# Kernel optimization log

Measured on AMD Instinct MI355X. Metric: run time of the kernel, lower is better.

The kernel has to match this reference:

```python
import jax, jax.numpy as jnp
import numpy as np

B, S, D = 8, 4096, 512      # batch, seq_len, input_dim
H = 2048                    # expert hidden dim
O = 512                     # expert_output_dim
E = 8                       # num_experts
TOP_K = 1


def setup_inputs() -> dict:
    key = jax.random.key(0)
    ks = jax.random.split(key, 8)
    sc = 0.02
    return {
        "x": jax.random.normal(ks[0], (B, S, D), dtype=jnp.float32),
        "Wr": jax.random.normal(ks[1], (D, E), dtype=jnp.float32) * sc,
        "br": jnp.zeros((E,), dtype=jnp.float32),
        "W1": jax.random.normal(ks[2], (E, D, H), dtype=jnp.float32) * sc,
        "b1": jnp.zeros((E, H), dtype=jnp.float32),
        "W2": jax.random.normal(ks[3], (E, H, O), dtype=jnp.float32) * sc,
        "b2": jnp.zeros((E, O), dtype=jnp.float32),
    }


def reference(x, Wr, br, W1, b1, W2, b2):
    b, s, d = x.shape
    xf = x.reshape(-1, d)                                   # [T, D]
    router_logits = xf @ Wr + br                            # [T, E]
    topk_logits, topk_idx = jax.lax.top_k(router_logits, TOP_K)  # [T, K]
    topk_gates = jax.nn.softmax(topk_logits, axis=1)        # [T, K] (ones for K=1)

    out = jnp.zeros((xf.shape[0], O), dtype=x.dtype)
    for k in range(TOP_K):
        idx_k = topk_idx[:, k]                              # [T]
        gate_k = topk_gates[:, k:k + 1]                     # [T, 1]
        # loop over the small fixed expert set; mask-combine per token
        for e in range(E):
            h = jax.nn.relu(xf @ W1[e] + b1[e])             # [T, H]
            oe = h @ W2[e] + b2[e]                          # [T, O]
            mask = (idx_k == e)[:, None]                    # [T, 1]
            out = out + jnp.where(mask, gate_k * oe, 0.0)
    return out.reshape(b, s, O)
```

## Files before the change

### kernel.cpp

```cpp
#include <hip/hip_runtime.h>
#include <stdint.h>

#define N_TOK 32768
#define D_IN  512
#define H_DIM 2048
#define O_DIM 512
#define N_EXP 8
#define NTILES 272
#define TPX    34

typedef __bf16 bf16x8 __attribute__((ext_vector_type(8)));
typedef float  f32x4  __attribute__((ext_vector_type(4)));
typedef unsigned int u32x4 __attribute__((ext_vector_type(4)));

struct alignas(8) us4 { unsigned short x, y, z, w; };

#define FENCE() asm volatile("" ::: "memory")
#define BAR()   do { FENCE(); __builtin_amdgcn_s_barrier(); FENCE(); } while (0)
#define WAITV0  asm volatile("s_waitcnt vmcnt(0)" ::: "memory")

__device__ __forceinline__ unsigned short f2bf(float f) {
  union { float f; unsigned u; } v; v.f = f;
  unsigned r = v.u + 0x7FFFu + ((v.u >> 16) & 1u);
  return (unsigned short)(r >> 16);
}

__device__ __forceinline__ void gll16(const void* src, void* lds_dst) {
  __builtin_amdgcn_global_load_lds(
      (const __attribute__((address_space(1))) void*)src,
      (__attribute__((address_space(3))) void*)lds_dst, 16, 0, 0);
}

__global__ void k_init(int* counts) {
  if (threadIdx.x < N_EXP) counts[threadIdx.x] = 0;
}

__global__ void k_transpose(const float* __restrict__ W, unsigned short* __restrict__ WT,
                            int R, int C) {
  __shared__ unsigned short tile[64][72];
  int e = blockIdx.y;
  const float* src = W + (size_t)e * R * C;
  unsigned short* dst = WT + (size_t)e * R * C;
  int tilesC = C >> 6;
  int tc = (blockIdx.x % tilesC) << 6;
  int tr = (blockIdx.x / tilesC) << 6;
  int tid = threadIdx.x;
  int rq = tid >> 4;
  int cq = tid & 15;
#pragma unroll
  for (int q = 0; q < 4; ++q) {
    int r = q * 16 + rq;
    float4 v = *(const float4*)(src + (size_t)(tr + r) * C + tc + cq * 4);
    us4 b;
    b.x = f2bf(v.x); b.y = f2bf(v.y); b.z = f2bf(v.z); b.w = f2bf(v.w);
    *(us4*)&tile[r][cq * 4] = b;
  }
  __syncthreads();
#pragma unroll
  for (int q = 0; q < 4; ++q) {
    int cc = q * 16 + rq;
    int rr = cq * 4;
    us4 o;
    o.x = tile[rr + 0][cc]; o.y = tile[rr + 1][cc];
    o.z = tile[rr + 2][cc]; o.w = tile[rr + 3][cc];
    *(us4*)(dst + (size_t)(tc + cc) * R + tr + rr) = o;
  }
}

__global__ void k_router(const float* __restrict__ x, const float* __restrict__ Wr,
                         const float* __restrict__ br, int* __restrict__ expert_id,
                         unsigned short* __restrict__ xbf) {
  int token = blockIdx.x * 4 + (threadIdx.x >> 6);
  int lane  = threadIdx.x & 63;
  const float* xr = x + (size_t)token * D_IN;
  float acc[N_EXP];
#pragma unroll
  for (int e = 0; e < N_EXP; ++e) acc[e] = 0.f;
#pragma unroll
  for (int j = 0; j < 2; ++j) {
    int i0 = lane * 8 + j * 4;
    float4 xv = *(const float4*)(xr + i0);
    us4 bb;
    bb.x = f2bf(xv.x); bb.y = f2bf(xv.y); bb.z = f2bf(xv.z); bb.w = f2bf(xv.w);
    *(us4*)(xbf + (size_t)token * D_IN + i0) = bb;
    float xs[4] = {xv.x, xv.y, xv.z, xv.w};
#pragma unroll
    for (int u = 0; u < 4; ++u) {
      const float4* wr = (const float4*)(Wr + (size_t)(i0 + u) * N_EXP);
      float4 w0 = wr[0], w1 = wr[1];
      acc[0] += xs[u] * w0.x; acc[1] += xs[u] * w0.y;
      acc[2] += xs[u] * w0.z; acc[3] += xs[u] * w0.w;
      acc[4] += xs[u] * w1.x; acc[5] += xs[u] * w1.y;
      acc[6] += xs[u] * w1.z; acc[7] += xs[u] * w1.w;
    }
  }
#pragma unroll
  for (int off = 32; off > 0; off >>= 1) {
#pragma unroll
    for (int e = 0; e < N_EXP; ++e) acc[e] += __shfl_xor(acc[e], off, 64);
  }
  if (lane == 0) {
    float best = acc[0] + br[0]; int bi = 0;
#pragma unroll
    for (int e = 1; e < N_EXP; ++e) {
      float v = acc[e] + br[e];
      if (v > best) { best = v; bi = e; }
    }
    expert_id[token] = bi;
  }
}

__global__ void k_count(const int* __restrict__ expert_id, int* __restrict__ counts) {
  __shared__ int lcnt[N_EXP];
  int tid = threadIdx.x;
  if (tid < N_EXP) lcnt[tid] = 0;
  __syncthreads();
  int e = expert_id[blockIdx.x * 1024 + tid];
  atomicAdd(&lcnt[e], 1);
  __syncthreads();
  if (tid < N_EXP) atomicAdd(&counts[tid], lcnt[tid]);
}

__global__ void k_scan(const int* __restrict__ counts, int* __restrict__ offsets,
                       int* __restrict__ cursor, int2* __restrict__ table) {
  int i = threadIdx.x;
  int s = 0, ts = 0, myexp = -1, myt = -1;
#pragma unroll
  for (int e = 0; e < N_EXP; ++e) {
    int c = counts[e];
    int tc = (c + 127) >> 7;
    if (i == e) { offsets[e] = s; cursor[e] = s; }
    if (i >= ts && i < ts + tc) { myexp = e; myt = i - ts; }
    s += c; ts += tc;
  }
  if (i < NTILES) table[i] = make_int2(myexp, myt);
}

__global__ void k_scatter(const int* __restrict__ expert_id, int* __restrict__ cursor,
                          int* __restrict__ idx_list) {
  __shared__ int lcnt[N_EXP], lbase[N_EXP];
  int tid = threadIdx.x;
  int i = blockIdx.x * 512 + tid;
  if (tid < N_EXP) lcnt[tid] = 0;
  __syncthreads();
  int e = expert_id[i];
  int lpos = atomicAdd(&lcnt[e], 1);
  __syncthreads();
  if (tid < N_EXP) lbase[tid] = atomicAdd(&cursor[tid], lcnt[tid]);
  __syncthreads();
  idx_list[lbase[e] + lpos] = i;
}


__launch_bounds__(256, 4)
__global__ void k_gemm1(const unsigned short* __restrict__ xbf,
                        const unsigned short* __restrict__ W1T,
                        const float* __restrict__ b1,
                        const int* __restrict__ counts, const int* __restrict__ offsets,
                        const int2* __restrict__ table, const int* __restrict__ idx_list,
                        unsigned short* __restrict__ Hperm,
                        int nt1, int ch, int hchunk) {
  int xcd = blockIdx.x & 7;
  int s   = blockIdx.x >> 3;
  int tile  = xcd * TPX + s / nt1;
  int ntile = s % nt1;
  int2 et = table[tile];
  int e = et.x;
  if (e < 0) return;
  int base   = offsets[e] + et.y * 128;
  int mvalid = min(128, counts[e] - et.y * 128);

  __shared__ __align__(16) unsigned char lds[32768];

  int tid = threadIdx.x, w = tid >> 6, lane = tid & 63;
  int l15 = lane & 15, l4 = lane >> 4;
  int wr = w >> 1, wc = w & 1;
  int n0 = ch * hchunk + ntile * 128;

  unsigned offA[4], offB[4];
#pragma unroll
  for (int q = 0; q < 4; ++q) {
    int d   = q * 4096 + w * 1024 + lane * 16;
    int row = d >> 7;
    int bs  = (d & 127) ^ ((row & 7) << 4);
    int tok = idx_list[base + min(row, mvalid - 1)];
    offA[q] = (unsigned)tok * (D_IN * 2) + bs;
    offB[q] = (unsigned)(e * H_DIM + n0 + row) * (D_IN * 2) + bs;
  }

  f32x4 acc[4][4];
#pragma unroll
  for (int a = 0; a < 4; ++a)
#pragma unroll
    for (int b = 0; b < 4; ++b) acc[a][b] = (f32x4){0.f, 0.f, 0.f, 0.f};

#define STAGE1(kstep) do {                                                   \
    unsigned kb = (unsigned)(kstep) * 128u;                                  \
    _Pragma("unroll")                                                        \
    for (int q = 0; q < 4; ++q) {                                            \
      gll16((const char*)xbf + offA[q] + kb, lds + q * 4096 + w * 1024);     \
      gll16((const char*)W1T + offB[q] + kb, lds + 16384 + q * 4096 + w * 1024); \
    }                                                                        \
  } while (0)

#define COMPUTE1() do {                                                      \
    const unsigned char* A = lds;                                            \
    const unsigned char* B = lds + 16384;                                    \
    __builtin_amdgcn_s_setprio(1);                                           \
    _Pragma("unroll")                                                        \
    for (int ks = 0; ks < 2; ++ks) {                                         \
      int kb = ks * 64 + l4 * 16;                                            \
      bf16x8 bfr[4];                                                         \
      _Pragma("unroll")                                                      \
      for (int nf = 0; nf < 4; ++nf) {                                       \
        int n = wc * 64 + nf * 16 + l15;                                     \
        bfr[nf] = *(const bf16x8*)(B + n * 128 + (kb ^ ((n & 7) << 4)));     \
      }                                                                      \
      _Pragma("unroll")                                                      \
      for (int mf = 0; mf < 4; ++mf) {                                       \
        int m = wr * 64 + mf * 16 + l15;                                     \
        bf16x8 af = *(const bf16x8*)(A + m * 128 + (kb ^ ((m & 7) << 4)));   \
        _Pragma("unroll")                                                    \
        for (int nf = 0; nf < 4; ++nf)                                       \
          acc[mf][nf] = __builtin_amdgcn_mfma_f32_16x16x32_bf16(af, bfr[nf], acc[mf][nf], 0, 0, 0); \
      }                                                                      \
    }                                                                        \
    __builtin_amdgcn_s_setprio(0);                                           \
  } while (0)

  const int NK = D_IN / 64;
  for (int t = 0; t < NK; ++t) {
    STAGE1(t);
    WAITV0;
    BAR();
    COMPUTE1();
    BAR();
  }

#pragma unroll
  for (int nf = 0; nf < 4; ++nf) {
    int col = wc * 64 + nf * 16 + l15;
    float bv = b1[(size_t)e * H_DIM + n0 + col];
#pragma unroll
    for (int mf = 0; mf < 4; ++mf) {
#pragma unroll
      for (int j = 0; j < 4; ++j) {
        int row = wr * 64 + mf * 16 + l4 * 4 + j;
        float v = fmaxf(acc[mf][nf][j] + bv, 0.f);
        *(unsigned short*)(lds + row * 256 + ((col * 2) ^ ((row & 7) << 4))) = f2bf(v);
      }
    }
  }
  BAR();
  {
    int row = tid >> 1;
    int seg = (tid & 1) * 128;
    if (row < mvalid) {
      int swz = (row & 7) << 4;
      char* gdst = (char*)Hperm + ((size_t)(base + row) * hchunk + ntile * 128) * 2 + seg;
      const unsigned char* lsrc = lds + row * 256;
#pragma unroll
      for (int i = 0; i < 8; ++i) {
        u32x4 v = *(const u32x4*)(lsrc + ((seg + i * 16) ^ swz));
        *(u32x4*)(gdst + i * 16) = v;
      }
    }
  }
#undef STAGE1
#undef COMPUTE1
}

__launch_bounds__(256, 4)
__global__ void k_gemm2(const unsigned short* __restrict__ Hperm,
                        const unsigned short* __restrict__ W2T,
                        const float* __restrict__ b2,
                        const int* __restrict__ counts, const int* __restrict__ offsets,
                        const int2* __restrict__ table, const int* __restrict__ idx_list,
                        float* __restrict__ out,
                        int ch, int hchunk, int accumulate) {
  int xcd = blockIdx.x & 7;
  int s   = blockIdx.x >> 3;
  int tile  = xcd * TPX + (s >> 2);
  int ntile = s & 3;
  int2 et = table[tile];
  int e = et.x;
  if (e < 0) return;
  int base   = offsets[e] + et.y * 128;
  int mvalid = min(128, counts[e] - et.y * 128);

  __shared__ __align__(16) unsigned char lds[32768];

  int tid = threadIdx.x, w = tid >> 6, lane = tid & 63;
  int l15 = lane & 15, l4 = lane >> 4;
  int wr = w >> 1, wc = w & 1;
  int o0 = ntile * 128;
  const unsigned hrow = (unsigned)hchunk * 2;

  unsigned offA[4], offB[4];
#pragma unroll
  for (int q = 0; q < 4; ++q) {
    int d   = q * 4096 + w * 1024 + lane * 16;
    int row = d >> 7;
    int bs  = (d & 127) ^ ((row & 7) << 4);
    offA[q] = (unsigned)min(base + row, N_TOK - 1) * hrow + bs;
    offB[q] = (unsigned)(e * O_DIM + o0 + row) * (H_DIM * 2) + (unsigned)ch * hchunk * 2 + bs;
  }

  f32x4 acc[4][4];
#pragma unroll
  for (int a = 0; a < 4; ++a)
#pragma unroll
    for (int b = 0; b < 4; ++b) acc[a][b] = (f32x4){0.f, 0.f, 0.f, 0.f};

#define STAGE2(kstep) do {                                                   \
    unsigned kb = (unsigned)(kstep) * 128u;                                  \
    _Pragma("unroll")                                                        \
    for (int q = 0; q < 4; ++q) {                                            \
      gll16((const char*)Hperm + offA[q] + kb, lds + q * 4096 + w * 1024);   \
      gll16((const char*)W2T   + offB[q] + kb, lds + 16384 + q * 4096 + w * 1024); \
    }                                                                        \
  } while (0)

#define COMPUTE2() do {                                                      \
    const unsigned char* A = lds;                                            \
    const unsigned char* B = lds + 16384;                                    \
    __builtin_amdgcn_s_setprio(1);                                           \
    _Pragma("unroll")                                                        \
    for (int ks = 0; ks < 2; ++ks) {                                         \
      int kb = ks * 64 + l4 * 16;                                            \
      bf16x8 bfr[4];                                                         \
      _Pragma("unroll")                                                      \
      for (int nf = 0; nf < 4; ++nf) {                                       \
        int n = wc * 64 + nf * 16 + l15;                                     \
        bfr[nf] = *(const bf16x8*)(B + n * 128 + (kb ^ ((n & 7) << 4)));     \
      }                                                                      \
      _Pragma("unroll")                                                      \
      for (int mf = 0; mf < 4; ++mf) {                                       \
        int m = wr * 64 + mf * 16 + l15;                                     \
        bf16x8 af = *(const bf16x8*)(A + m * 128 + (kb ^ ((m & 7) << 4)));   \
        _Pragma("unroll")                                                    \
        for (int nf = 0; nf < 4; ++nf)                                       \
          acc[mf][nf] = __builtin_amdgcn_mfma_f32_16x16x32_bf16(af, bfr[nf], acc[mf][nf], 0, 0, 0); \
      }                                                                      \
    }                                                                        \
    __builtin_amdgcn_s_setprio(0);                                           \
  } while (0)

  const int NK = hchunk / 64;
  for (int t = 0; t < NK; ++t) {
    STAGE2(t);
    WAITV0;
    BAR();
    COMPUTE2();
    BAR();
  }

#pragma unroll
  for (int nf = 0; nf < 4; ++nf) {
    int o = o0 + wc * 64 + nf * 16 + l15;
    float bv = b2[(size_t)e * O_DIM + o];
#pragma unroll
    for (int mf = 0; mf < 4; ++mf) {
#pragma unroll
      for (int j = 0; j < 4; ++j) {
        int row = wr * 64 + mf * 16 + l4 * 4 + j;
        if (row < mvalid) {
          int tok = idx_list[base + row];
          float* p = out + (size_t)tok * O_DIM + o;
          if (accumulate) *p = *p + acc[mf][nf][j];
          else            *p = acc[mf][nf][j] + bv;
        }
      }
    }
  }
#undef STAGE2
#undef COMPUTE2
}

extern "C" void kernel_launch(void* const* d_in, const int* in_sizes, int n_in,
                              void* d_out, int out_size, void* d_ws, size_t ws_size,
                              hipStream_t stream) {
  const float* x  = (const float*)d_in[0];
  const float* Wr = (const float*)d_in[1];
  const float* br = (const float*)d_in[2];
  const float* W1 = (const float*)d_in[3];
  const float* b1 = (const float*)d_in[4];
  const float* W2 = (const float*)d_in[5];
  const float* b2 = (const float*)d_in[6];
  float* out = (float*)d_out;

  char* ws = (char*)d_ws;
  int*  counts    = (int*)(ws + 0);
  int*  offsets   = (int*)(ws + 64);
  int*  cursor    = (int*)(ws + 128);
  int2* table     = (int2*)(ws + 256);
  int*  expert_id = (int*)(ws + 4096);
  int*  idx_list  = (int*)(ws + 4096 + N_TOK * 4);
  size_t off = 4096 + 2 * (size_t)N_TOK * 4;
  unsigned short* xbf = (unsigned short*)(ws + off);
  off += (size_t)N_TOK * D_IN * 2;
  unsigned short* W1T = (unsigned short*)(ws + off);
  off += (size_t)N_EXP * H_DIM * D_IN * 2;
  unsigned short* W2T = (unsigned short*)(ws + off);
  off += (size_t)N_EXP * H_DIM * O_DIM * 2;
  unsigned short* Hperm = (unsigned short*)(ws + off);

  int hchunk = 2048;
  while (hchunk > 256 && off + (size_t)N_TOK * hchunk * 2 > ws_size) hchunk >>= 1;
  int nch = H_DIM / hchunk;
  int nt1 = hchunk / 128;

  k_init<<<1, 64, 0, stream>>>(counts);
  k_transpose<<<dim3(256, N_EXP), 256, 0, stream>>>(W1, W1T, D_IN, H_DIM);
  k_transpose<<<dim3(256, N_EXP), 256, 0, stream>>>(W2, W2T, H_DIM, O_DIM);
  k_router<<<N_TOK / 4, 256, 0, stream>>>(x, Wr, br, expert_id, xbf);
  k_count<<<N_TOK / 1024, 1024, 0, stream>>>(expert_id, counts);
  k_scan<<<1, 512, 0, stream>>>(counts, offsets, cursor, table);
  k_scatter<<<N_TOK / 512, 512, 0, stream>>>(expert_id, cursor, idx_list);

  for (int ch = 0; ch < nch; ++ch) {
    k_gemm1<<<8 * TPX * nt1, 256, 0, stream>>>(xbf, W1T, b1, counts, offsets,
                                               table, idx_list, Hperm, nt1, ch, hchunk);
    k_gemm2<<<8 * TPX * 4, 256, 0, stream>>>(Hperm, W2T, b2, counts, offsets,
                                             table, idx_list, out, ch, hchunk, ch > 0);
  }
}
```

Baseline: 332.3 us.

## Double-buffer LDS tiles with K=32 phases to overlap loads with MFMA

Both expert GEMM kernels now split the 32 KB LDS into two ping-pong buffers of K=32 slices. Each phase issues the next slice's global-to-LDS loads before waiting with vmcnt(4) on the current one, so memory latency overlaps MFMA work instead of stalling on vmcnt(0) every step. The swizzle changes to match 64-byte rows, and launch bounds rise to 5 blocks per CU. The cost is twice as many barrier pairs per K, since each phase is half as long, and possible register pressure from the higher occupancy target.

```diff
diff --git a/kernel.cpp b/kernel.cpp
--- a/kernel.cpp
+++ b/kernel.cpp
@@ -17,6 +17,7 @@
 
 #define FENCE() asm volatile("" ::: "memory")
 #define BAR()   do { FENCE(); __builtin_amdgcn_s_barrier(); FENCE(); } while (0)
+#define WAITV4  asm volatile("s_waitcnt vmcnt(4)" ::: "memory")
 #define WAITV0  asm volatile("s_waitcnt vmcnt(0)" ::: "memory")
 
 __device__ __forceinline__ unsigned short f2bf(float f) {
@@ -152,7 +153,7 @@
 }
 
 
-__launch_bounds__(256, 4)
+__launch_bounds__(256, 5)
 __global__ void k_gemm1(const unsigned short* __restrict__ xbf,
                         const unsigned short* __restrict__ W1T,
                         const float* __restrict__ b1,
@@ -177,15 +178,15 @@
   int wr = w >> 1, wc = w & 1;
   int n0 = ch * hchunk + ntile * 128;
 
-  unsigned offA[4], offB[4];
-#pragma unroll
-  for (int q = 0; q < 4; ++q) {
-    int d   = q * 4096 + w * 1024 + lane * 16;
-    int row = d >> 7;
-    int bs  = (d & 127) ^ ((row & 7) << 4);
+  unsigned offA[2], offB[2];
+#pragma unroll
+  for (int i = 0; i < 2; ++i) {
+    int d   = i * 4096 + w * 1024 + lane * 16;
+    int row = d >> 6;
+    int cs  = (d & 63) ^ ((row & 3) << 4);
     int tok = idx_list[base + min(row, mvalid - 1)];
-    offA[q] = (unsigned)tok * (D_IN * 2) + bs;
-    offB[q] = (unsigned)(e * H_DIM + n0 + row) * (D_IN * 2) + bs;
+    offA[i] = (unsigned)tok * (D_IN * 2) + cs;
+    offB[i] = (unsigned)(e * H_DIM + n0 + row) * (D_IN * 2) + cs;
   }
 
   f32x4 acc[4][4];
@@ -194,46 +195,43 @@
 #pragma unroll
     for (int b = 0; b < 4; ++b) acc[a][b] = (f32x4){0.f, 0.f, 0.f, 0.f};
 
-#define STAGE1(kstep) do {                                                   \
-    unsigned kb = (unsigned)(kstep) * 128u;                                  \
+#define STAGE1(j) do {                                                       \
+    unsigned kb = (unsigned)(j) * 64u;                                       \
+    unsigned sa = ((unsigned)(j) & 1u) * 8192u;                              \
+    gll16((const char*)xbf + offA[0] + kb, lds + sa + w * 1024);             \
+    gll16((const char*)xbf + offA[1] + kb, lds + sa + 4096 + w * 1024);      \
+    gll16((const char*)W1T + offB[0] + kb, lds + 16384 + sa + w * 1024);     \
+    gll16((const char*)W1T + offB[1] + kb, lds + 16384 + sa + 4096 + w * 1024); \
+  } while (0)
+
+#define COMPUTE1(j) do {                                                     \
+    const unsigned char* A = lds + ((unsigned)(j) & 1u) * 8192u;             \
+    const unsigned char* B = lds + 16384u + ((unsigned)(j) & 1u) * 8192u;    \
+    bf16x8 bfr[4];                                                           \
     _Pragma("unroll")                                                        \
-    for (int q = 0; q < 4; ++q) {                                            \
-      gll16((const char*)xbf + offA[q] + kb, lds + q * 4096 + w * 1024);     \
-      gll16((const char*)W1T + offB[q] + kb, lds + 16384 + q * 4096 + w * 1024); \
+    for (int nf = 0; nf < 4; ++nf) {                                         \
+      int n = wc * 64 + nf * 16 + l15;                                       \
+      bfr[nf] = *(const bf16x8*)(B + n * 64 + ((l4 * 16) ^ ((n & 3) << 4))); \
     }                                                                        \
-  } while (0)
-
-#define COMPUTE1() do {                                                      \
-    const unsigned char* A = lds;                                            \
-    const unsigned char* B = lds + 16384;                                    \
     __builtin_amdgcn_s_setprio(1);                                           \
     _Pragma("unroll")                                                        \
-    for (int ks = 0; ks < 2; ++ks) {                                         \
-      int kb = ks * 64 + l4 * 16;                                            \
-      bf16x8 bfr[4];                                                         \
+    for (int mf = 0; mf < 4; ++mf) {                                         \
+      int m = wr * 64 + mf * 16 + l15;                                       \
+      bf16x8 af = *(const bf16x8*)(A + m * 64 + ((l4 * 16) ^ ((m & 3) << 4))); \
       _Pragma("unroll")                                                      \
-      for (int nf = 0; nf < 4; ++nf) {                                       \
-        int n = wc * 64 + nf * 16 + l15;                                     \
-        bfr[nf] = *(const bf16x8*)(B + n * 128 + (kb ^ ((n & 7) << 4)));     \
-      }                                                                      \
-      _Pragma("unroll")                                                      \
-      for (int mf = 0; mf < 4; ++mf) {                                       \
-        int m = wr * 64 + mf * 16 + l15;                                     \
-        bf16x8 af = *(const bf16x8*)(A + m * 128 + (kb ^ ((m & 7) << 4)));   \
-        _Pragma("unroll")                                                    \
-        for (int nf = 0; nf < 4; ++nf)                                       \
-          acc[mf][nf] = __builtin_amdgcn_mfma_f32_16x16x32_bf16(af, bfr[nf], acc[mf][nf], 0, 0, 0); \
-      }                                                                      \
+      for (int nf = 0; nf < 4; ++nf)                                         \
+        acc[mf][nf] = __builtin_amdgcn_mfma_f32_16x16x32_bf16(af, bfr[nf], acc[mf][nf], 0, 0, 0); \
     }                                                                        \
     __builtin_amdgcn_s_setprio(0);                                           \
   } while (0)
 
-  const int NK = D_IN / 64;
-  for (int t = 0; t < NK; ++t) {
-    STAGE1(t);
-    WAITV0;
+  const int NPH = D_IN / 32;
+  STAGE1(0);
+  for (int j = 0; j < NPH; ++j) {
+    if (j + 1 < NPH) { STAGE1(j + 1); WAITV4; }
+    else             { WAITV0; }
     BAR();
-    COMPUTE1();
+    COMPUTE1(j);
     BAR();
   }
 
@@ -270,7 +268,7 @@
 #undef COMPUTE1
 }
 
-__launch_bounds__(256, 4)
+__launch_bounds__(256, 5)
 __global__ void k_gemm2(const unsigned short* __restrict__ Hperm,
                         const unsigned short* __restrict__ W2T,
                         const float* __restrict__ b2,
@@ -296,14 +294,14 @@
   int o0 = ntile * 128;
   const unsigned hrow = (unsigned)hchunk * 2;
 
-  unsigned offA[4], offB[4];
-#pragma unroll
-  for (int q = 0; q < 4; ++q) {
-    int d   = q * 4096 + w * 1024 + lane * 16;
-    int row = d >> 7;
-    int bs  = (d & 127) ^ ((row & 7) << 4);
-    offA[q] = (unsigned)min(base + row, N_TOK - 1) * hrow + bs;
-    offB[q] = (unsigned)(e * O_DIM + o0 + row) * (H_DIM * 2) + (unsigned)ch * hchunk * 2 + bs;
+  unsigned offA[2], offB[2];
+#pragma unroll
+  for (int i = 0; i < 2; ++i) {
+    int d   = i * 4096 + w * 1024 + lane * 16;
+    int row = d >> 6;
+    int cs  = (d & 63) ^ ((row & 3) << 4);
+    offA[i] = (unsigned)min(base + row, N_TOK - 1) * hrow + cs;
+    offB[i] = (unsigned)(e * O_DIM + o0 + row) * (H_DIM * 2) + (unsigned)ch * hchunk * 2 + cs;
   }
 
   f32x4 acc[4][4];
@@ -312,46 +310,43 @@
 #pragma unroll
     for (int b = 0; b < 4; ++b) acc[a][b] = (f32x4){0.f, 0.f, 0.f, 0.f};
 
-#define STAGE2(kstep) do {                                                   \
-    unsigned kb = (unsigned)(kstep) * 128u;                                  \
+#define STAGE2(j) do {                                                       \
+    unsigned kb = (unsigned)(j) * 64u;                                       \
+    unsigned sa = ((unsigned)(j) & 1u) * 8192u;                              \
+    gll16((const char*)Hperm + offA[0] + kb, lds + sa + w * 1024);           \
+    gll16((const char*)Hperm + offA[1] + kb, lds + sa + 4096 + w * 1024);    \
+    gll16((const char*)W2T   + offB[0] + kb, lds + 16384 + sa + w * 1024);   \
+    gll16((const char*)W2T   + offB[1] + kb, lds + 16384 + sa + 4096 + w * 1024); \
+  } while (0)
+
+#define COMPUTE2(j) do {                                                     \
+    const unsigned char* A = lds + ((unsigned)(j) & 1u) * 8192u;             \
+    const unsigned char* B = lds + 16384u + ((unsigned)(j) & 1u) * 8192u;    \
+    bf16x8 bfr[4];                                                           \
     _Pragma("unroll")                                                        \
-    for (int q = 0; q < 4; ++q) {                                            \
-      gll16((const char*)Hperm + offA[q] + kb, lds + q * 4096 + w * 1024);   \
-      gll16((const char*)W2T   + offB[q] + kb, lds + 16384 + q * 4096 + w * 1024); \
+    for (int nf = 0; nf < 4; ++nf) {                                         \
+      int n = wc * 64 + nf * 16 + l15;                                       \
+      bfr[nf] = *(const bf16x8*)(B + n * 64 + ((l4 * 16) ^ ((n & 3) << 4))); \
     }                                                                        \
-  } while (0)
-
-#define COMPUTE2() do {                                                      \
-    const unsigned char* A = lds;                                            \
-    const unsigned char* B = lds + 16384;                                    \
     __builtin_amdgcn_s_setprio(1);                                           \
     _Pragma("unroll")                                                        \
-    for (int ks = 0; ks < 2; ++ks) {                                         \
-      int kb = ks * 64 + l4 * 16;                                            \
-      bf16x8 bfr[4];                                                         \
+    for (int mf = 0; mf < 4; ++mf) {                                         \
+      int m = wr * 64 + mf * 16 + l15;                                       \
+      bf16x8 af = *(const bf16x8*)(A + m * 64 + ((l4 * 16) ^ ((m & 3) << 4))); \
       _Pragma("unroll")                                                      \
-      for (int nf = 0; nf < 4; ++nf) {                                       \
-        int n = wc * 64 + nf * 16 + l15;                                     \
-        bfr[nf] = *(const bf16x8*)(B + n * 128 + (kb ^ ((n & 7) << 4)));     \
-      }                                                                      \
-      _Pragma("unroll")                                                      \
-      for (int mf = 0; mf < 4; ++mf) {                                       \
-        int m = wr * 64 + mf * 16 + l15;                                     \
-        bf16x8 af = *(const bf16x8*)(A + m * 128 + (kb ^ ((m & 7) << 4)));   \
-        _Pragma("unroll")                                                    \
-        for (int nf = 0; nf < 4; ++nf)                                       \
-          acc[mf][nf] = __builtin_amdgcn_mfma_f32_16x16x32_bf16(af, bfr[nf], acc[mf][nf], 0, 0, 0); \
-      }                                                                      \
+      for (int nf = 0; nf < 4; ++nf)                                         \
+        acc[mf][nf] = __builtin_amdgcn_mfma_f32_16x16x32_bf16(af, bfr[nf], acc[mf][nf], 0, 0, 0); \
     }                                                                        \
     __builtin_amdgcn_s_setprio(0);                                           \
   } while (0)
 
-  const int NK = hchunk / 64;
-  for (int t = 0; t < NK; ++t) {
-    STAGE2(t);
-    WAITV0;
+  const int NPH = hchunk / 32;
+  STAGE2(0);
+  for (int j = 0; j < NPH; ++j) {
+    if (j + 1 < NPH) { STAGE2(j + 1); WAITV4; }
+    else             { WAITV0; }
     BAR();
-    COMPUTE2();
+    COMPUTE2(j);
     BAR();
   }
 
```

After: 463.7 us. +39.5%, slower.

## Widen expert GEMM tiles to 128x256 with one wave per column strip

Applied to the files above, without the earlier changes.

Both expert GEMM kernels move from 128x128 output tiles to 128x256 tiles. Each of the four waves now owns a full 128-row by 64-column strip with 8x4 MFMA accumulators, so A-fragment LDS reads are reused across more N and fewer blocks re-stage the same token rows. LDS grows to 48 KB and occupancy is lowered to 3 blocks per CU. The GEMM1 epilogue writes out in two halves through the reused LDS buffer. The cost is higher register pressure, lower occupancy and half as many blocks in the grid.

```diff
diff --git a/kernel.cpp b/kernel.cpp
--- a/kernel.cpp
+++ b/kernel.cpp
@@ -152,7 +152,7 @@
 }
 
 
-__launch_bounds__(256, 4)
+__launch_bounds__(256, 3)
 __global__ void k_gemm1(const unsigned short* __restrict__ xbf,
                         const unsigned short* __restrict__ W1T,
                         const float* __restrict__ b1,
@@ -170,14 +170,14 @@
   int base   = offsets[e] + et.y * 128;
   int mvalid = min(128, counts[e] - et.y * 128);
 
-  __shared__ __align__(16) unsigned char lds[32768];
+  __shared__ __align__(16) unsigned char lds[49152];
 
   int tid = threadIdx.x, w = tid >> 6, lane = tid & 63;
   int l15 = lane & 15, l4 = lane >> 4;
-  int wr = w >> 1, wc = w & 1;
-  int n0 = ch * hchunk + ntile * 128;
-
-  unsigned offA[4], offB[4];
+  int wc = w;
+  int n0 = ch * hchunk + ntile * 256;
+
+  unsigned offA[4], offB[8];
 #pragma unroll
   for (int q = 0; q < 4; ++q) {
     int d   = q * 4096 + w * 1024 + lane * 16;
@@ -185,22 +185,29 @@
     int bs  = (d & 127) ^ ((row & 7) << 4);
     int tok = idx_list[base + min(row, mvalid - 1)];
     offA[q] = (unsigned)tok * (D_IN * 2) + bs;
+  }
+#pragma unroll
+  for (int q = 0; q < 8; ++q) {
+    int d   = q * 4096 + w * 1024 + lane * 16;
+    int row = d >> 7;
+    int bs  = (d & 127) ^ ((row & 7) << 4);
     offB[q] = (unsigned)(e * H_DIM + n0 + row) * (D_IN * 2) + bs;
   }
 
-  f32x4 acc[4][4];
-#pragma unroll
-  for (int a = 0; a < 4; ++a)
+  f32x4 acc[8][4];
+#pragma unroll
+  for (int a = 0; a < 8; ++a)
 #pragma unroll
     for (int b = 0; b < 4; ++b) acc[a][b] = (f32x4){0.f, 0.f, 0.f, 0.f};
 
 #define STAGE1(kstep) do {                                                   \
     unsigned kb = (unsigned)(kstep) * 128u;                                  \
     _Pragma("unroll")                                                        \
-    for (int q = 0; q < 4; ++q) {                                            \
+    for (int q = 0; q < 4; ++q)                                              \
       gll16((const char*)xbf + offA[q] + kb, lds + q * 4096 + w * 1024);     \
+    _Pragma("unroll")                                                        \
+    for (int q = 0; q < 8; ++q)                                              \
       gll16((const char*)W1T + offB[q] + kb, lds + 16384 + q * 4096 + w * 1024); \
-    }                                                                        \
   } while (0)
 
 #define COMPUTE1() do {                                                      \
@@ -217,8 +224,8 @@
         bfr[nf] = *(const bf16x8*)(B + n * 128 + (kb ^ ((n & 7) << 4)));     \
       }                                                                      \
       _Pragma("unroll")                                                      \
-      for (int mf = 0; mf < 4; ++mf) {                                       \
-        int m = wr * 64 + mf * 16 + l15;                                     \
+      for (int mf = 0; mf < 8; ++mf) {                                       \
+        int m = mf * 16 + l15;                                               \
         bf16x8 af = *(const bf16x8*)(A + m * 128 + (kb ^ ((m & 7) << 4)));   \
         _Pragma("unroll")                                                    \
         for (int nf = 0; nf < 4; ++nf)                                       \
@@ -237,27 +244,35 @@
     BAR();
   }
 
-#pragma unroll
-  for (int nf = 0; nf < 4; ++nf) {
-    int col = wc * 64 + nf * 16 + l15;
-    float bv = b1[(size_t)e * H_DIM + n0 + col];
-#pragma unroll
-    for (int mf = 0; mf < 4; ++mf) {
-#pragma unroll
-      for (int j = 0; j < 4; ++j) {
-        int row = wr * 64 + mf * 16 + l4 * 4 + j;
-        float v = fmaxf(acc[mf][nf][j] + bv, 0.f);
-        *(unsigned short*)(lds + row * 256 + ((col * 2) ^ ((row & 7) << 4))) = f2bf(v);
+  float bv[4];
+#pragma unroll
+  for (int nf = 0; nf < 4; ++nf)
+    bv[nf] = b1[(size_t)e * H_DIM + n0 + wc * 64 + nf * 16 + l15];
+
+#pragma unroll
+  for (int h = 0; h < 2; ++h) {
+    BAR();
+    if ((wc >> 1) == h) {
+#pragma unroll
+      for (int nf = 0; nf < 4; ++nf) {
+        int colh = (wc & 1) * 64 + nf * 16 + l15;
+#pragma unroll
+        for (int mf = 0; mf < 8; ++mf) {
+#pragma unroll
+          for (int j = 0; j < 4; ++j) {
+            int row = mf * 16 + l4 * 4 + j;
+            float v = fmaxf(acc[mf][nf][j] + bv[nf], 0.f);
+            *(unsigned short*)(lds + row * 256 + ((colh * 2) ^ ((row & 7) << 4))) = f2bf(v);
+          }
+        }
       }
     }
-  }
-  BAR();
-  {
+    BAR();
     int row = tid >> 1;
     int seg = (tid & 1) * 128;
     if (row < mvalid) {
       int swz = (row & 7) << 4;
-      char* gdst = (char*)Hperm + ((size_t)(base + row) * hchunk + ntile * 128) * 2 + seg;
+      char* gdst = (char*)Hperm + ((size_t)(base + row) * hchunk + ntile * 256 + h * 128) * 2 + seg;
       const unsigned char* lsrc = lds + row * 256;
 #pragma unroll
       for (int i = 0; i < 8; ++i) {
@@ -270,7 +285,7 @@
 #undef COMPUTE1
 }
 
-__launch_bounds__(256, 4)
+__launch_bounds__(256, 3)
 __global__ void k_gemm2(const unsigned short* __restrict__ Hperm,
                         const unsigned short* __restrict__ W2T,
                         const float* __restrict__ b2,
@@ -280,45 +295,52 @@
                         int ch, int hchunk, int accumulate) {
   int xcd = blockIdx.x & 7;
   int s   = blockIdx.x >> 3;
-  int tile  = xcd * TPX + (s >> 2);
-  int ntile = s & 3;
+  int tile  = xcd * TPX + (s >> 1);
+  int ntile = s & 1;
   int2 et = table[tile];
   int e = et.x;
   if (e < 0) return;
   int base   = offsets[e] + et.y * 128;
   int mvalid = min(128, counts[e] - et.y * 128);
 
-  __shared__ __align__(16) unsigned char lds[32768];
+  __shared__ __align__(16) unsigned char lds[49152];
 
   int tid = threadIdx.x, w = tid >> 6, lane = tid & 63;
   int l15 = lane & 15, l4 = lane >> 4;
-  int wr = w >> 1, wc = w & 1;
-  int o0 = ntile * 128;
+  int wc = w;
+  int o0 = ntile * 256;
   const unsigned hrow = (unsigned)hchunk * 2;
 
-  unsigned offA[4], offB[4];
+  unsigned offA[4], offB[8];
 #pragma unroll
   for (int q = 0; q < 4; ++q) {
     int d   = q * 4096 + w * 1024 + lane * 16;
     int row = d >> 7;
     int bs  = (d & 127) ^ ((row & 7) << 4);
     offA[q] = (unsigned)min(base + row, N_TOK - 1) * hrow + bs;
+  }
+#pragma unroll
+  for (int q = 0; q < 8; ++q) {
+    int d   = q * 4096 + w * 1024 + lane * 16;
+    int row = d >> 7;
+    int bs  = (d & 127) ^ ((row & 7) << 4);
     offB[q] = (unsigned)(e * O_DIM + o0 + row) * (H_DIM * 2) + (unsigned)ch * hchunk * 2 + bs;
   }
 
-  f32x4 acc[4][4];
-#pragma unroll
-  for (int a = 0; a < 4; ++a)
+  f32x4 acc[8][4];
+#pragma unroll
+  for (int a = 0; a < 8; ++a)
 #pragma unroll
     for (int b = 0; b < 4; ++b) acc[a][b] = (f32x4){0.f, 0.f, 0.f, 0.f};
 
 #define STAGE2(kstep) do {                                                   \
     unsigned kb = (unsigned)(kstep) * 128u;                                  \
     _Pragma("unroll")                                                        \
-    for (int q = 0; q < 4; ++q) {                                            \
+    for (int q = 0; q < 4; ++q)                                              \
       gll16((const char*)Hperm + offA[q] + kb, lds + q * 4096 + w * 1024);   \
-      gll16((const char*)W2T   + offB[q] + kb, lds + 16384 + q * 4096 + w * 1024); \
-    }                                                                        \
+    _Pragma("unroll")                                                        \
+    for (int q = 0; q < 8; ++q)                                              \
+      gll16((const char*)W2T + offB[q] + kb, lds + 16384 + q * 4096 + w * 1024); \
   } while (0)
 
 #define COMPUTE2() do {                                                      \
@@ -335,8 +357,8 @@
         bfr[nf] = *(const bf16x8*)(B + n * 128 + (kb ^ ((n & 7) << 4)));     \
       }                                                                      \
       _Pragma("unroll")                                                      \
-      for (int mf = 0; mf < 4; ++mf) {                                       \
-        int m = wr * 64 + mf * 16 + l15;                                     \
+      for (int mf = 0; mf < 8; ++mf) {                                       \
+        int m = mf * 16 + l15;                                               \
         bf16x8 af = *(const bf16x8*)(A + m * 128 + (kb ^ ((m & 7) << 4)));   \
         _Pragma("unroll")                                                    \
         for (int nf = 0; nf < 4; ++nf)                                       \
@@ -358,17 +380,17 @@
 #pragma unroll
   for (int nf = 0; nf < 4; ++nf) {
     int o = o0 + wc * 64 + nf * 16 + l15;
-    float bv = b2[(size_t)e * O_DIM + o];
-#pragma unroll
-    for (int mf = 0; mf < 4; ++mf) {
+    float bvv = b2[(size_t)e * O_DIM + o];
+#pragma unroll
+    for (int mf = 0; mf < 8; ++mf) {
 #pragma unroll
       for (int j = 0; j < 4; ++j) {
-        int row = wr * 64 + mf * 16 + l4 * 4 + j;
+        int row = mf * 16 + l4 * 4 + j;
         if (row < mvalid) {
           int tok = idx_list[base + row];
           float* p = out + (size_t)tok * O_DIM + o;
           if (accumulate) *p = *p + acc[mf][nf][j];
-          else            *p = acc[mf][nf][j] + bv;
+          else            *p = acc[mf][nf][j] + bvv;
         }
       }
     }
@@ -408,7 +430,7 @@
   int hchunk = 2048;
   while (hchunk > 256 && off + (size_t)N_TOK * hchunk * 2 > ws_size) hchunk >>= 1;
   int nch = H_DIM / hchunk;
-  int nt1 = hchunk / 128;
+  int nt1 = hchunk / 256;
 
   k_init<<<1, 64, 0, stream>>>(counts);
   k_transpose<<<dim3(256, N_EXP), 256, 0, stream>>>(W1, W1T, D_IN, H_DIM);
@@ -421,7 +443,7 @@
   for (int ch = 0; ch < nch; ++ch) {
     k_gemm1<<<8 * TPX * nt1, 256, 0, stream>>>(xbf, W1T, b1, counts, offsets,
                                                table, idx_list, Hperm, nt1, ch, hchunk);
-    k_gemm2<<<8 * TPX * 4, 256, 0, stream>>>(Hperm, W2T, b2, counts, offsets,
+    k_gemm2<<<8 * TPX * 2, 256, 0, stream>>>(Hperm, W2T, b2, counts, offsets,
                                              table, idx_list, out, ch, hchunk, ch > 0);
   }
 }
```

Result: slower. 437.1 us (+31.5%).

## Pipeline both expert GEMMs with 4-slot LDS ring and 512-thread blocks

Applied to the files above, without the earlier changes.

Both grouped GEMM kernels now use 512-thread blocks, with 8 waves each covering a 64x32 sub-tile, and a 4-slot LDS ring buffer of 128 KB. Global-to-LDS loads run three k-steps ahead, guarded by partial vmcnt waits, which removes the per-step full drain and the second barrier. The aim is to overlap memory latency with MFMA work. In exchange, LDS use limits occupancy to one block per CU, and each wave holds fewer accumulators.

```diff
diff --git a/kernel.cpp b/kernel.cpp
--- a/kernel.cpp
+++ b/kernel.cpp
@@ -8,6 +8,7 @@
 #define N_EXP 8
 #define NTILES 272
 #define TPX    34
+#define SLOT   32768u
 
 typedef __bf16 bf16x8 __attribute__((ext_vector_type(8)));
 typedef float  f32x4  __attribute__((ext_vector_type(4)));
@@ -17,6 +18,8 @@
 
 #define FENCE() asm volatile("" ::: "memory")
 #define BAR()   do { FENCE(); __builtin_amdgcn_s_barrier(); FENCE(); } while (0)
+#define WAITV8  asm volatile("s_waitcnt vmcnt(8)" ::: "memory")
+#define WAITV4  asm volatile("s_waitcnt vmcnt(4)" ::: "memory")
 #define WAITV0  asm volatile("s_waitcnt vmcnt(0)" ::: "memory")
 
 __device__ __forceinline__ unsigned short f2bf(float f) {
@@ -152,7 +155,7 @@
 }
 
 
-__launch_bounds__(256, 4)
+__launch_bounds__(512, 1)
 __global__ void k_gemm1(const unsigned short* __restrict__ xbf,
                         const unsigned short* __restrict__ W1T,
                         const float* __restrict__ b1,
@@ -170,17 +173,17 @@
   int base   = offsets[e] + et.y * 128;
   int mvalid = min(128, counts[e] - et.y * 128);
 
-  __shared__ __align__(16) unsigned char lds[32768];
+  __shared__ __align__(16) unsigned char lds[4][SLOT];
 
   int tid = threadIdx.x, w = tid >> 6, lane = tid & 63;
   int l15 = lane & 15, l4 = lane >> 4;
-  int wr = w >> 1, wc = w & 1;
+  int wr = w >> 2, wc = w & 3;
   int n0 = ch * hchunk + ntile * 128;
 
-  unsigned offA[4], offB[4];
-#pragma unroll
-  for (int q = 0; q < 4; ++q) {
-    int d   = q * 4096 + w * 1024 + lane * 16;
+  unsigned offA[2], offB[2];
+#pragma unroll
+  for (int q = 0; q < 2; ++q) {
+    int d   = q * 8192 + w * 1024 + lane * 16;
     int row = d >> 7;
     int bs  = (d & 127) ^ ((row & 7) << 4);
     int tok = idx_list[base + min(row, mvalid - 1)];
@@ -188,79 +191,86 @@
     offB[q] = (unsigned)(e * H_DIM + n0 + row) * (D_IN * 2) + bs;
   }
 
-  f32x4 acc[4][4];
+  f32x4 acc[4][2];
 #pragma unroll
   for (int a = 0; a < 4; ++a)
 #pragma unroll
-    for (int b = 0; b < 4; ++b) acc[a][b] = (f32x4){0.f, 0.f, 0.f, 0.f};
-
-#define STAGE1(kstep) do {                                                   \
-    unsigned kb = (unsigned)(kstep) * 128u;                                  \
+    for (int b = 0; b < 2; ++b) acc[a][b] = (f32x4){0.f, 0.f, 0.f, 0.f};
+
+#define STAGE1(t) do {                                                       \
+    unsigned kb = (unsigned)(t) * 128u;                                      \
+    unsigned char* sl = lds[(t) & 3];                                        \
     _Pragma("unroll")                                                        \
-    for (int q = 0; q < 4; ++q) {                                            \
-      gll16((const char*)xbf + offA[q] + kb, lds + q * 4096 + w * 1024);     \
-      gll16((const char*)W1T + offB[q] + kb, lds + 16384 + q * 4096 + w * 1024); \
+    for (int q = 0; q < 2; ++q) {                                            \
+      gll16((const char*)xbf + offA[q] + kb, sl + q * 8192 + w * 1024);      \
+      gll16((const char*)W1T + offB[q] + kb, sl + 16384 + q * 8192 + w * 1024); \
     }                                                                        \
   } while (0)
 
-#define COMPUTE1() do {                                                      \
-    const unsigned char* A = lds;                                            \
-    const unsigned char* B = lds + 16384;                                    \
+#define COMPUTE1(t) do {                                                     \
+    const unsigned char* A = lds[(t) & 3];                                   \
+    const unsigned char* B = A + 16384;                                      \
     __builtin_amdgcn_s_setprio(1);                                           \
     _Pragma("unroll")                                                        \
     for (int ks = 0; ks < 2; ++ks) {                                         \
       int kb = ks * 64 + l4 * 16;                                            \
-      bf16x8 bfr[4];                                                         \
+      bf16x8 bfr[2];                                                         \
       _Pragma("unroll")                                                      \
-      for (int nf = 0; nf < 4; ++nf) {                                       \
-        int n = wc * 64 + nf * 16 + l15;                                     \
+      for (int nf = 0; nf < 2; ++nf) {                                       \
+        int n = wc * 32 + nf * 16 + l15;                                     \
         bfr[nf] = *(const bf16x8*)(B + n * 128 + (kb ^ ((n & 7) << 4)));     \
       }                                                                      \
       _Pragma("unroll")                                                      \
       for (int mf = 0; mf < 4; ++mf) {                                       \
         int m = wr * 64 + mf * 16 + l15;                                     \
         bf16x8 af = *(const bf16x8*)(A + m * 128 + (kb ^ ((m & 7) << 4)));   \
-        _Pragma("unroll")                                                    \
-        for (int nf = 0; nf < 4; ++nf)                                       \
-          acc[mf][nf] = __builtin_amdgcn_mfma_f32_16x16x32_bf16(af, bfr[nf], acc[mf][nf], 0, 0, 0); \
+        acc[mf][0] = __builtin_amdgcn_mfma_f32_16x16x32_bf16(af, bfr[0], acc[mf][0], 0, 0, 0); \
+        acc[mf][1] = __builtin_amdgcn_mfma_f32_16x16x32_bf16(af, bfr[1], acc[mf][1], 0, 0, 0); \
       }                                                                      \
     }                                                                        \
     __builtin_amdgcn_s_setprio(0);                                           \
   } while (0)
 
   const int NK = D_IN / 64;
+  STAGE1(0); STAGE1(1); STAGE1(2);
   for (int t = 0; t < NK; ++t) {
-    STAGE1(t);
-    WAITV0;
+    int rem = NK - 1 - t;
+    if (rem >= 2)      { WAITV8; }
+    else if (rem == 1) { WAITV4; }
+    else               { WAITV0; }
     BAR();
-    COMPUTE1();
-    BAR();
-  }
-
-#pragma unroll
-  for (int nf = 0; nf < 4; ++nf) {
-    int col = wc * 64 + nf * 16 + l15;
-    float bv = b1[(size_t)e * H_DIM + n0 + col];
+    if (t + 3 < NK) STAGE1(t + 3);
+    COMPUTE1(t);
+  }
+  BAR();
+
+  float bv[2];
+#pragma unroll
+  for (int nf = 0; nf < 2; ++nf)
+    bv[nf] = b1[(size_t)e * H_DIM + n0 + wc * 32 + nf * 16 + l15];
+#pragma unroll
+  for (int nf = 0; nf < 2; ++nf) {
+    int col = wc * 32 + nf * 16 + l15;
 #pragma unroll
     for (int mf = 0; mf < 4; ++mf) {
 #pragma unroll
       for (int j = 0; j < 4; ++j) {
         int row = wr * 64 + mf * 16 + l4 * 4 + j;
-        float v = fmaxf(acc[mf][nf][j] + bv, 0.f);
-        *(unsigned short*)(lds + row * 256 + ((col * 2) ^ ((row & 7) << 4))) = f2bf(v);
+        float v = fmaxf(acc[mf][nf][j] + bv[nf], 0.f);
+        *(unsigned short*)(&lds[0][0] + row * 256 + ((col * 2) ^ ((row & 7) << 4))) = f2bf(v);
       }
     }
   }
   BAR();
   {
-    int row = tid >> 1;
-    int seg = (tid & 1) * 128;
+    int row = tid >> 2;
+    int seg = (tid & 3) * 64;
     if (row < mvalid) {
       int swz = (row & 7) << 4;
       char* gdst = (char*)Hperm + ((size_t)(base + row) * hchunk + ntile * 128) * 2 + seg;
-      const unsigned char* lsrc = lds + row * 256;
-#pragma unroll
-      for (int i = 0; i < 8; ++i) {
+      const unsigned char* lsrc = &lds[0][0] + row * 256;
+#pragma unroll
+      for (int i = 0; i < 4; ++i) {
         u32x4 v = *(const u32x4*)(lsrc + ((seg + i * 16) ^ swz));
         *(u32x4*)(gdst + i * 16) = v;
       }
@@ -270,7 +280,7 @@
 #undef COMPUTE1
 }
 
-__launch_bounds__(256, 4)
+__launch_bounds__(512, 1)
 __global__ void k_gemm2(const unsigned short* __restrict__ Hperm,
                         const unsigned short* __restrict__ W2T,
                         const float* __restrict__ b2,
@@ -288,77 +298,80 @@
   int base   = offsets[e] + et.y * 128;
   int mvalid = min(128, counts[e] - et.y * 128);
 
-  __shared__ __align__(16) unsigned char lds[32768];
+  __shared__ __align__(16) unsigned char lds[4][SLOT];
 
   int tid = threadIdx.x, w = tid >> 6, lane = tid & 63;
   int l15 = lane & 15, l4 = lane >> 4;
-  int wr = w >> 1, wc = w & 1;
+  int wr = w >> 2, wc = w & 3;
   int o0 = ntile * 128;
   const unsigned hrow = (unsigned)hchunk * 2;
 
-  unsigned offA[4], offB[4];
-#pragma unroll
-  for (int q = 0; q < 4; ++q) {
-    int d   = q * 4096 + w * 1024 + lane * 16;
+  unsigned offA[2], offB[2];
+#pragma unroll
+  for (int q = 0; q < 2; ++q) {
+    int d   = q * 8192 + w * 1024 + lane * 16;
     int row = d >> 7;
     int bs  = (d & 127) ^ ((row & 7) << 4);
     offA[q] = (unsigned)min(base + row, N_TOK - 1) * hrow + bs;
     offB[q] = (unsigned)(e * O_DIM + o0 + row) * (H_DIM * 2) + (unsigned)ch * hchunk * 2 + bs;
   }
 
-  f32x4 acc[4][4];
+  f32x4 acc[4][2];
 #pragma unroll
   for (int a = 0; a < 4; ++a)
 #pragma unroll
-    for (int b = 0; b < 4; ++b) acc[a][b] = (f32x4){0.f, 0.f, 0.f, 0.f};
-
-#define STAGE2(kstep) do {                                                   \
-    unsigned kb = (unsigned)(kstep) * 128u;                                  \
+    for (int b = 0; b < 2; ++b) acc[a][b] = (f32x4){0.f, 0.f, 0.f, 0.f};
+
+#define STAGE2(t) do {                                                       \
+    unsigned kb = (unsigned)(t) * 128u;                                      \
+    unsigned char* sl = lds[(t) & 3];                                        \
     _Pragma("unroll")                                                        \
-    for (int q = 0; q < 4; ++q) {                                            \
-      gll16((const char*)Hperm + offA[q] + kb, lds + q * 4096 + w * 1024);   \
-      gll16((const char*)W2T   + offB[q] + kb, lds + 16384 + q * 4096 + w * 1024); \
+    for (int q = 0; q < 2; ++q) {                                            \
+      gll16((const char*)Hperm + offA[q] + kb, sl + q * 8192 + w * 1024);    \
+      gll16((const char*)W2T   + offB[q] + kb, sl + 16384 + q * 8192 + w * 1024); \
     }                                                                        \
   } while (0)
 
-#define COMPUTE2() do {                                                      \
-    const unsigned char* A = lds;                                            \
-    const unsigned char* B = lds + 16384;                                    \
+#define COMPUTE2(t) do {                                                     \
+    const unsigned char* A = lds[(t) & 3];                                   \
+    const unsigned char* B = A + 16384;                                      \
     __builtin_amdgcn_s_setprio(1);                                           \
     _Pragma("unroll")                                                        \
     for (int ks = 0; ks < 2; ++ks) {                                         \
       int kb = ks * 64 + l4 * 16;                                            \
-      bf16x8 bfr[4];                                                         \
+      bf16x8 bfr[2];                                                         \
       _Pragma("unroll")                                                      \
-      for (int nf = 0; nf < 4; ++nf) {                                       \
-        int n = wc * 64 + nf * 16 + l15;                                     \
+      for (int nf = 0; nf < 2; ++nf) {                                       \
+        int n = wc * 32 + nf * 16 + l15;                                     \
         bfr[nf] = *(const bf16x8*)(B + n * 128 + (kb ^ ((n & 7) << 4)));     \
       }                                                                      \
       _Pragma("unroll")                                                      \
       for (int mf = 0; mf < 4; ++mf) {                                       \
         int m = wr * 64 + mf * 16 + l15;                                     \
         bf16x8 af = *(const bf16x8*)(A + m * 128 + (kb ^ ((m & 7) << 4)));   \
-        _Pragma("unroll")                                                    \
-        for (int nf = 0; nf < 4; ++nf)                                       \
-          acc[mf][nf] = __builtin_amdgcn_mfma_f32_16x16x32_bf16(af, bfr[nf], acc[mf][nf], 0, 0, 0); \
+        acc[mf][0] = __builtin_amdgcn_mfma_f32_16x16x32_bf16(af, bfr[0], acc[mf][0], 0, 0, 0); \
+        acc[mf][1] = __builtin_amdgcn_mfma_f32_16x16x32_bf16(af, bfr[1], acc[mf][1], 0, 0, 0); \
       }                                                                      \
     }                                                                        \
     __builtin_amdgcn_s_setprio(0);                                           \
   } while (0)
 
   const int NK = hchunk / 64;
+  STAGE2(0); STAGE2(1); STAGE2(2);
   for (int t = 0; t < NK; ++t) {
-    STAGE2(t);
-    WAITV0;
+    int rem = NK - 1 - t;
+    if (rem >= 2)      { WAITV8; }
+    else if (rem == 1) { WAITV4; }
+    else               { WAITV0; }
     BAR();
-    COMPUTE2();
-    BAR();
-  }
-
-#pragma unroll
-  for (int nf = 0; nf < 4; ++nf) {
-    int o = o0 + wc * 64 + nf * 16 + l15;
-    float bv = b2[(size_t)e * O_DIM + o];
+    if (t + 3 < NK) STAGE2(t + 3);
+    COMPUTE2(t);
+  }
+
+#pragma unroll
+  for (int nf = 0; nf < 2; ++nf) {
+    int o = o0 + wc * 32 + nf * 16 + l15;
+    float bvv = b2[(size_t)e * O_DIM + o];
 #pragma unroll
     for (int mf = 0; mf < 4; ++mf) {
 #pragma unroll
@@ -368,7 +381,7 @@
           int tok = idx_list[base + row];
           float* p = out + (size_t)tok * O_DIM + o;
           if (accumulate) *p = *p + acc[mf][nf][j];
-          else            *p = acc[mf][nf][j] + bv;
+          else            *p = acc[mf][nf][j] + bvv;
         }
       }
     }
@@ -419,9 +432,9 @@
   k_scatter<<<N_TOK / 512, 512, 0, stream>>>(expert_id, cursor, idx_list);
 
   for (int ch = 0; ch < nch; ++ch) {
-    k_gemm1<<<8 * TPX * nt1, 256, 0, stream>>>(xbf, W1T, b1, counts, offsets,
+    k_gemm1<<<8 * TPX * nt1, 512, 0, stream>>>(xbf, W1T, b1, counts, offsets,
                                                table, idx_list, Hperm, nt1, ch, hchunk);
-    k_gemm2<<<8 * TPX * 4, 256, 0, stream>>>(Hperm, W2T, b2, counts, offsets,
+    k_gemm2<<<8 * TPX * 4, 512, 0, stream>>>(Hperm, W2T, b2, counts, offsets,
                                              table, idx_list, out, ch, hchunk, ch > 0);
   }
 }
```

After: 383.6 us. 15.5% more time.
